# Kernel optimization log

Hardware: AMD Instinct MI355X
Metric: run time of the kernel (lower is better)

## Reference

```python
import jax, jax.numpy as jnp
import numpy as np

N, E = 50000, 800000
IN_F, OUT_F, EMB, KER = 64, 64, 3, 4


def setup_inputs() -> dict:
    key = jax.random.key(0)
    ks = jax.random.split(key, 6)
    x = jax.random.normal(ks[0], (N, IN_F), dtype=jnp.float32)
    edge_idx = jax.random.randint(ks[1], (2, E), 0, N, dtype=jnp.int64)
    spec_domain = jax.random.normal(ks[2], (N, EMB), dtype=jnp.float32)
    weight = 0.1 * jax.random.normal(ks[3], (IN_F, OUT_F, KER), dtype=jnp.float32)
    bias_p = 0.1 * jax.random.normal(ks[4], (OUT_F,), dtype=jnp.float32)
    mu = 0.005 * jax.random.normal(ks[5], (EMB, KER), dtype=jnp.float32)
    sig = jnp.ones((1, KER), dtype=jnp.float32)  # repo default 60140 underflows exp with random embeddings
    return {"x": x, "edge_idx": edge_idx, "spec_domain": spec_domain,
            "weight": weight, "bias_p": bias_p, "mu": mu, "sig": sig}


def reference(x, edge_idx, spec_domain, weight, bias_p, mu, sig):
    n = x.shape[0]
    row, col = edge_idx[0], edge_idx[1]
    # support for all kernels at once: [N, out, K]
    support = jnp.einsum('ni,iok->nok', x, weight)
    # per-edge Gaussian kernel values: [E, K]
    diff = spec_domain[row] - spec_domain[col]               # [E, emb]
    dm = diff[:, :, None] - mu[None, :, :]                   # [E, emb, K]
    qq = -0.5 * jnp.sum(dm * dm, axis=1)                     # [E, K]
    value = jnp.exp(sig[0][None, :] * qq)                    # [E, K]
    # sparse mm: out[row] += value * support[col], per kernel
    msgs = value[:, None, :] * support[col]                  # [E, out, K]
    out = jax.ops.segment_sum(msgs, row, num_segments=n)     # [N, out, K]
    return out.sum(axis=2) + bias_p
```

## Files before the change

### kernel.cpp

```cpp
#include <hip/hip_runtime.h>
#include <hip/hip_fp16.h>

#define FIN 64
#define CAP 48
#define BINSH 8
#define NBINMAX 256
#define PCAP 5120
#define TILE_B 2048

__global__ __launch_bounds__(256) void p1_kernel(const float* __restrict__ x,
                                                 const float* __restrict__ weight,
                                                 __half* __restrict__ sup,
                                                 const int* __restrict__ eidx,
                                                 int* __restrict__ gcur,
                                                 int* __restrict__ part,
                                                 int n, int e_total, int sblocks) {
    const int t = threadIdx.x;
    __shared__ int hist[NBINMAX], lbase[NBINMAX], gbase[NBINMAX];
    __shared__ int wsum[4];

    {
        const int lane = t & 63;
        const int wid  = t >> 6;
        const int r0 = __builtin_amdgcn_readfirstlane(blockIdx.x * 32 + wid * 8);
        if (r0 + 7 < n) {
            const float* __restrict__ xr = x + (size_t)r0 * 64;

            float4 acc[8];
            #pragma unroll
            for (int r = 0; r < 8; ++r) acc[r] = make_float4(0.f, 0.f, 0.f, 0.f);

            #pragma unroll 4
            for (int ic = 0; ic < 16; ++ic) {
                float4 w0 = *(const float4*)&weight[(ic * 4 + 0) * 256 + lane * 4];
                float4 w1 = *(const float4*)&weight[(ic * 4 + 1) * 256 + lane * 4];
                float4 w2 = *(const float4*)&weight[(ic * 4 + 2) * 256 + lane * 4];
                float4 w3 = *(const float4*)&weight[(ic * 4 + 3) * 256 + lane * 4];
                #pragma unroll
                for (int r = 0; r < 8; ++r) {
                    float4 xv = *(const float4*)&xr[r * 64 + ic * 4];
                    acc[r].x += xv.x * w0.x + xv.y * w1.x + xv.z * w2.x + xv.w * w3.x;
                    acc[r].y += xv.x * w0.y + xv.y * w1.y + xv.z * w2.y + xv.w * w3.y;
                    acc[r].z += xv.x * w0.z + xv.y * w1.z + xv.z * w2.z + xv.w * w3.z;
                    acc[r].w += xv.x * w0.w + xv.y * w1.w + xv.z * w2.w + xv.w * w3.w;
                }
            }

            #pragma unroll
            for (int r = 0; r < 8; ++r) {
                union { __half2 h[2]; uint2 u; } p;
                p.h[0] = __floats2half2_rn(acc[r].x, acc[r].y);
                p.h[1] = __floats2half2_rn(acc[r].z, acc[r].w);
                *(uint2*)&sup[(size_t)(r0 + r) * 256 + lane * 4] = p.u;
            }
        }
    }

    if (blockIdx.x < sblocks) {
        int nz = 0;
        #pragma unroll
        for (int j = 1; j < 16; j += 2) nz |= eidx[j];
        const int is64 = (nz == 0);

        hist[t] = 0;
        __syncthreads();

        const int base = blockIdx.x * TILE_B;
        int nv = e_total - base;
        if (nv > TILE_B) nv = TILE_B;
        if (nv < 0) nv = 0;

        int er[8], ec_[8], lp[8], vb[8];
        #pragma unroll
        for (int i = 0; i < 4; ++i) {
            const int pl = t + 256 * i;
            const int pg = (base >> 1) + pl;
            int r0 = 0, c0 = 0, r1 = 0, c1 = 0, v0 = 0, v1 = 0;
            if (2 * pl < nv) {
                if (is64) {
                    int4 rr = ((const int4*)eidx)[pg];
                    int4 cc = ((const int4*)(eidx + 2 * (size_t)e_total))[pg];
                    r0 = rr.x; c0 = cc.x; v0 = 1;
                    if (2 * pl + 1 < nv) { r1 = rr.z; c1 = cc.z; v1 = 1; }
                } else {
                    int2 rr = ((const int2*)eidx)[pg];
                    int2 cc = ((const int2*)(eidx + (size_t)e_total))[pg];
                    r0 = rr.x; c0 = cc.x; v0 = 1;
                    if (2 * pl + 1 < nv) { r1 = rr.y; c1 = cc.y; v1 = 1; }
                }
            }
            er[2 * i] = r0; ec_[2 * i] = c0; vb[2 * i] = v0;
            er[2 * i + 1] = r1; ec_[2 * i + 1] = c1; vb[2 * i + 1] = v1;
        }
        #pragma unroll
        for (int i = 0; i < 8; ++i) {
            lp[i] = vb[i] ? atomicAdd(&hist[er[i] >> BINSH], 1) : 0;
        }
        __syncthreads();

        {
            const int lane = t & 63;
            const int w = t >> 6;
            int h = hist[t];
            int s = h;
            #pragma unroll
            for (int off = 1; off < 64; off <<= 1) {
                int u = __shfl_up(s, off, 64);
                if (lane >= off) s += u;
            }
            if (lane == 63) wsum[w] = s;
            __syncthreads();
            if (t == 0) {
                int a = 0;
                #pragma unroll
                for (int q = 0; q < 4; ++q) { int u = wsum[q]; wsum[q] = a; a += u; }
            }
            __syncthreads();
            lbase[t] = s - h + wsum[w];
            gbase[t] = (h > 0) ? atomicAdd(&gcur[t], h) : 0;
        }
        __syncthreads();

        #pragma unroll
        for (int i = 0; i < 8; ++i) {
            if (vb[i]) {
                int b = er[i] >> BINSH;
                int dst = gbase[b] + lp[i];
                if (dst < PCAP) part[b * PCAP + dst] = (ec_[i] << 8) | (er[i] & 255);
            }
        }
    }
}

__global__ __launch_bounds__(1024) void p2_kernel(const int* __restrict__ gcur,
                                                  const int* __restrict__ part,
                                                  const float* __restrict__ spec,
                                                  const float* __restrict__ mu,
                                                  const float* __restrict__ sig,
                                                  int* __restrict__ cnt,
                                                  int* __restrict__ scol,
                                                  uint2* __restrict__ sval, int n) {
    __shared__ int cl[256];
    const int t = threadIdx.x;
    const int b = blockIdx.x;
    const int row0 = b << BINSH;
    if (t < 256) cl[t] = 0;
    __syncthreads();

    float m0[4], m1[4], m2[4], sg[4];
    #pragma unroll
    for (int k = 0; k < 4; ++k) {
        m0[k] = mu[k]; m1[k] = mu[4 + k]; m2[k] = mu[8 + k]; sg[k] = sig[k];
    }

    int nloc = gcur[b];
    if (nloc > PCAP) nloc = PCAP;
    const int* __restrict__ mypart = part + b * PCAP;

    for (int i = t; i < nloc; i += 1024) {
        int e = mypart[i];
        int rl = e & 255;
        int col = ((unsigned)e) >> 8;
        int row = row0 + rl;

        float d0 = spec[row * 3 + 0] - spec[col * 3 + 0];
        float d1 = spec[row * 3 + 1] - spec[col * 3 + 1];
        float d2 = spec[row * 3 + 2] - spec[col * 3 + 2];
        float v[4];
        #pragma unroll
        for (int k = 0; k < 4; ++k) {
            float a = d0 - m0[k], bb = d1 - m1[k], c = d2 - m2[k];
            v[k] = __expf(sg[k] * (-0.5f * (a * a + bb * bb + c * c)));
        }
        union { __half2 h; unsigned u; } p01, p23;
        p01.h = __floats2half2_rn(v[0], v[1]);
        p23.h = __floats2half2_rn(v[2], v[3]);

        int pos = atomicAdd(&cl[rl], 1);
        if (pos < CAP) {
            scol[(size_t)row * CAP + pos] = col;
            sval[(size_t)row * CAP + pos] = make_uint2(p01.u, p23.u);
        }
    }
    __syncthreads();

    int row = row0 + t;
    if (t < 256 && row < n) cnt[row] = (cl[t] > CAP) ? CAP : cl[t];
}

__device__ __forceinline__ float dot_supv(uint2 p, uint2 pv) {
    float2 f0 = __half22float2(__builtin_bit_cast(__half2, p.x));
    float2 f1 = __half22float2(__builtin_bit_cast(__half2, p.y));
    float2 a0 = __half22float2(__builtin_bit_cast(__half2, pv.x));
    float2 a1 = __half22float2(__builtin_bit_cast(__half2, pv.y));
    return f0.x * a0.x + f0.y * a0.y + f1.x * a1.x + f1.y * a1.y;
}

__global__ __launch_bounds__(256, 6) void row_kernel(const int* __restrict__ cnt,
                                                     const int* __restrict__ scol,
                                                     const uint2* __restrict__ sval,
                                                     const __half* __restrict__ sup,
                                                     const float* __restrict__ bias,
                                                     float* __restrict__ out, int n) {
    const int lane = threadIdx.x & 63;
    const int wl = threadIdx.x >> 6;
    const int wv = __builtin_amdgcn_readfirstlane(blockIdx.x * 4 + wl);
    const int NW = gridDim.x * 4;
    const float bias_l = bias[lane];
    const unsigned un = (unsigned)n;

    for (int r = wv; r < n; r += NW) {
        int ec = cnt[r];
        if (ec > CAP) ec = CAP;
        const size_t base = (size_t)r * CAP;
        float acc = bias_l;

        for (int j = 0; j < ec; j += 16) {
            int c[16]; uint2 w[16];
            #pragma unroll
            for (int i = 0; i < 16; ++i) {
                int idx = j + i;
                int cc = scol[base + idx];
                uint2 ww = sval[base + idx];
                bool valid = idx < ec;
                c[i] = ((unsigned)cc < un) ? cc : 0;
                w[i] = valid ? ww : make_uint2(0u, 0u);
            }
            uint2 p[16];
            #pragma unroll
            for (int i = 0; i < 16; ++i)
                p[i] = *(const uint2*)(sup + ((size_t)c[i] * 256 + lane * 4));
            #pragma unroll
            for (int i = 0; i < 16; ++i)
                acc += dot_supv(p[i], w[i]);
        }
        out[(size_t)r * 64 + lane] = acc;
    }
}

extern "C" void kernel_launch(void* const* d_in, const int* in_sizes, int n_in,
                              void* d_out, int out_size, void* d_ws, size_t ws_size,
                              hipStream_t stream) {
    const float* x      = (const float*)d_in[0];
    const int*   eidx   = (const int*)d_in[1];
    const float* spec   = (const float*)d_in[2];
    const float* weight = (const float*)d_in[3];
    const float* bias   = (const float*)d_in[4];
    const float* mu     = (const float*)d_in[5];
    const float* sig    = (const float*)d_in[6];
    float* out = (float*)d_out;

    const int N = in_sizes[0] / FIN;
    const int E = in_sizes[1] / 2;
    const int NB32 = (N + 31) / 32;
    const int SBLK = (E + TILE_B - 1) / TILE_B;
    const int NBIN = (N + (1 << BINSH) - 1) >> BINSH;

    char* w = (char*)d_ws;
    size_t off = 0;
    int* gcur = (int*)(w + off);            off += NBINMAX * 4;
    __half* sup = (__half*)(w + off);       off += (size_t)N * 256 * sizeof(__half);
    off = (off + 255) & ~(size_t)255;
    int* cnt = (int*)(w + off);             off += (size_t)N * 4;
    off = (off + 255) & ~(size_t)255;
    int* scol = (int*)(w + off);            off += (size_t)N * CAP * 4;
    off = (off + 255) & ~(size_t)255;
    uint2* sval = (uint2*)(w + off);        off += (size_t)N * CAP * 8;
    off = (off + 255) & ~(size_t)255;
    int* part = (int*)(w + off);            off += (size_t)NBIN * PCAP * 4;

    hipMemsetAsync(gcur, 0, NBINMAX * 4, stream);
    p1_kernel<<<NB32, 256, 0, stream>>>(x, weight, sup, eidx, gcur, part, N, E, SBLK);
    p2_kernel<<<NBIN, 1024, 0, stream>>>(gcur, part, spec, mu, sig, cnt, scol, sval, N);
    row_kernel<<<1536, 256, 0, stream>>>(cnt, scol, sval, sup, bias, out, N);
}
```

Measured before the change: 122.6 us.

## Stage weights in LDS and double per-block edge tile in binning pass

```diff
diff --git a/kernel.cpp b/kernel.cpp
--- a/kernel.cpp
+++ b/kernel.cpp
@@ -6,7 +6,7 @@
 #define BINSH 8
 #define NBINMAX 256
 #define PCAP 5120
-#define TILE_B 2048
+#define TILE_B 4096
 
 __global__ __launch_bounds__(256) void p1_kernel(const float* __restrict__ x,
                                                  const float* __restrict__ weight,
@@ -16,8 +16,17 @@
                                                  int* __restrict__ part,
                                                  int n, int e_total, int sblocks) {
     const int t = threadIdx.x;
+    __shared__ float wlds[64 * 256];
     __shared__ int hist[NBINMAX], lbase[NBINMAX], gbase[NBINMAX];
     __shared__ int wsum[4];
+
+    {
+        const float4* __restrict__ w4 = (const float4*)weight;
+        float4* __restrict__ s4 = (float4*)wlds;
+        #pragma unroll
+        for (int j = 0; j < 16; ++j) s4[t + j * 256] = w4[t + j * 256];
+    }
+    __syncthreads();
 
     {
         const int lane = t & 63;
@@ -32,10 +41,10 @@
 
             #pragma unroll 4
             for (int ic = 0; ic < 16; ++ic) {
-                float4 w0 = *(const float4*)&weight[(ic * 4 + 0) * 256 + lane * 4];
-                float4 w1 = *(const float4*)&weight[(ic * 4 + 1) * 256 + lane * 4];
-                float4 w2 = *(const float4*)&weight[(ic * 4 + 2) * 256 + lane * 4];
-                float4 w3 = *(const float4*)&weight[(ic * 4 + 3) * 256 + lane * 4];
+                float4 w0 = *(const float4*)&wlds[(ic * 4 + 0) * 256 + lane * 4];
+                float4 w1 = *(const float4*)&wlds[(ic * 4 + 1) * 256 + lane * 4];
+                float4 w2 = *(const float4*)&wlds[(ic * 4 + 2) * 256 + lane * 4];
+                float4 w3 = *(const float4*)&wlds[(ic * 4 + 3) * 256 + lane * 4];
                 #pragma unroll
                 for (int r = 0; r < 8; ++r) {
                     float4 xv = *(const float4*)&xr[r * 64 + ic * 4];
@@ -70,9 +79,9 @@
         if (nv > TILE_B) nv = TILE_B;
         if (nv < 0) nv = 0;
 
-        int er[8], ec_[8], lp[8], vb[8];
-        #pragma unroll
-        for (int i = 0; i < 4; ++i) {
+        int pay[16], bn[16], lp[16];
+        #pragma unroll
+        for (int i = 0; i < 8; ++i) {
             const int pl = t + 256 * i;
             const int pg = (base >> 1) + pl;
             int r0 = 0, c0 = 0, r1 = 0, c1 = 0, v0 = 0, v1 = 0;
@@ -89,12 +98,14 @@
                     if (2 * pl + 1 < nv) { r1 = rr.y; c1 = cc.y; v1 = 1; }
                 }
             }
-            er[2 * i] = r0; ec_[2 * i] = c0; vb[2 * i] = v0;
-            er[2 * i + 1] = r1; ec_[2 * i + 1] = c1; vb[2 * i + 1] = v1;
-        }
-        #pragma unroll
-        for (int i = 0; i < 8; ++i) {
-            lp[i] = vb[i] ? atomicAdd(&hist[er[i] >> BINSH], 1) : 0;
+            pay[2 * i]     = (c0 << 8) | (r0 & 255);
+            bn[2 * i]      = v0 ? (r0 >> BINSH) : -1;
+            pay[2 * i + 1] = (c1 << 8) | (r1 & 255);
+            bn[2 * i + 1]  = v1 ? (r1 >> BINSH) : -1;
+        }
+        #pragma unroll
+        for (int i = 0; i < 16; ++i) {
+            lp[i] = (bn[i] >= 0) ? atomicAdd(&hist[bn[i]], 1) : 0;
         }
         __syncthreads();
 
@@ -122,11 +133,10 @@
         __syncthreads();
 
         #pragma unroll
-        for (int i = 0; i < 8; ++i) {
-            if (vb[i]) {
-                int b = er[i] >> BINSH;
-                int dst = gbase[b] + lp[i];
-                if (dst < PCAP) part[b * PCAP + dst] = (ec_[i] << 8) | (er[i] & 255);
+        for (int i = 0; i < 16; ++i) {
+            if (bn[i] >= 0) {
+                int dst = gbase[bn[i]] + lp[i];
+                if (dst < PCAP) part[bn[i] * PCAP + dst] = pay[i];
             }
         }
     }
```

After: 120.0 us. 1.02x faster.
